# Performance work log

Hardware: AMD Instinct MI355X
Metric: run time of the kernel (lower is better)

Reference implementation:

```python
import jax, jax.numpy as jnp
import numpy as np

B, N, H = 32, 2048, 256          # batch, num_docs, hidden_dim
F_HEADS = 8                      # config.dynamic_fusion_heads
NH = 8                           # num_heads inside each nn.MultiheadAttention
STEPS = 3                        # config.meta_adaptation_steps


def setup_inputs() -> dict:
    key = jax.random.key(0)
    ks = jax.random.split(key, 10)
    s = 0.02
    return {
        "query": jax.random.normal(ks[0], (B, H), jnp.float32),
        "retrieved_docs": jax.random.normal(ks[1], (B, N, H), jnp.float32),
        "causal_weights": jax.random.uniform(ks[2], (B, N, 1), jnp.float32),
        "context_history": jax.random.normal(ks[3], (B, H), jnp.float32),
        # per-fusion-head MultiheadAttention params (torch layout: in_proj [3H,H])
        "in_proj_w": jax.random.normal(ks[4], (F_HEADS, 3 * H, H), jnp.float32) * s,
        "in_proj_b": jnp.zeros((F_HEADS, 3 * H), jnp.float32),
        "out_proj_w": jax.random.normal(ks[5], (F_HEADS, H, H), jnp.float32) * s,
        "out_proj_b": jnp.zeros((F_HEADS, H), jnp.float32),
        "strategy_w": jax.random.normal(ks[6], (F_HEADS, H), jnp.float32) * s,
        "strategy_b": jnp.zeros((F_HEADS,), jnp.float32),
        "meta_params": jax.random.normal(ks[7], (STEPS, H, H), jnp.float32) * 0.02,
    }


def _mha_qlen1(q, kv, Wi, bi, Wo, bo):
    # q: [B,H] (query length 1), kv: [B,N,H]. Torch MHA semantics, batch_first.
    Wq, Wk, Wv = jnp.split(Wi, 3, axis=0)
    bq, bk, bv = jnp.split(bi, 3)
    dh = H // NH
    qh = (q @ Wq.T + bq).reshape(B, NH, dh)
    kh = (kv @ Wk.T + bk).reshape(B, N, NH, dh)
    vh = (kv @ Wv.T + bv).reshape(B, N, NH, dh)
    scores = jnp.einsum('bhd,bnhd->bhn', qh, kh) / jnp.sqrt(jnp.float32(dh))
    attn = jax.nn.softmax(scores, axis=-1)
    ctx = jnp.einsum('bhn,bnhd->bhd', attn, vh).reshape(B, H)
    return ctx @ Wo.T + bo


def reference(query, retrieved_docs, causal_weights, context_history,
              in_proj_w, in_proj_b, out_proj_w, out_proj_b,
              strategy_w, strategy_b, meta_params):
    # causal weighting of retrieved docs (shared across all fusion heads)
    weighted_docs = retrieved_docs * causal_weights  # [B,N,H]

    # batch all 8 fusion heads' cross-attention in one vmapped pass -> [F,B,H]
    heads_out = jax.vmap(
        lambda Wi, bi, Wo, bo: _mha_qlen1(query, weighted_docs, Wi, bi, Wo, bo)
    )(in_proj_w, in_proj_b, out_proj_w, out_proj_b)

    # sequential residual meta-adaptation steps (same matrices for every head)
    for i in range(STEPS):
        heads_out = heads_out + heads_out @ meta_params[i]

    # strategy-weighted combine of fusion heads
    strategy = jax.nn.softmax(query @ strategy_w.T + strategy_b, axis=-1)  # [B,F]
    return jnp.einsum('fbh,bf->bh', heads_out, strategy)  # [B,H]
```

## Files before the change

### kernel.cpp

```cpp
#include <hip/hip_runtime.h>
#include <hip/hip_bf16.h>


#define B_ 32
#define N_ 2048
#define H_ 256
#define F_ 8
#define FH_ 64
#define NCH_ 16
#define NCHK_ 2

typedef unsigned short u16;
typedef __attribute__((ext_vector_type(8))) short bf16x8;
typedef __attribute__((ext_vector_type(4))) float f32x4;
#define MFMA(a, b, c) __builtin_amdgcn_mfma_f32_16x16x32_bf16((a), (b), (c), 0, 0, 0)

__device__ __forceinline__ u16 f2b(float x) {
  unsigned u = __builtin_bit_cast(unsigned, x);
  return (u16)((u + 0x7fffu + ((u >> 16) & 1u)) >> 16);
}
__device__ __forceinline__ float b2f(u16 h) {
  unsigned u = ((unsigned)h) << 16;
  return __builtin_bit_cast(float, u);
}
__device__ __forceinline__ bf16x8 ld8b(const float* p) {
  float4 v0 = *(const float4*)p, v1 = *(const float4*)(p + 4);
  bf16x8 a;
  a[0] = f2b(v0.x); a[1] = f2b(v0.y); a[2] = f2b(v0.z); a[3] = f2b(v0.w);
  a[4] = f2b(v1.x); a[5] = f2b(v1.y); a[6] = f2b(v1.z); a[7] = f2b(v1.w);
  return a;
}

static constexpr size_t UB_U     = 0;
static constexpr size_t UB_W     = 1048576;
static constexpr size_t UB_L     = 3145728;
static constexpr size_t UB_STRAT = 3153920;
static constexpr size_t UB_MT    = 3154944;

#define SMEM_BYTES 52224

__device__ __forceinline__ void dev_k1(char* smem, int f, int hf, int bh,
    const float* __restrict__ query, const float* __restrict__ ipw,
    const float* __restrict__ ipb, const float* __restrict__ stw,
    const float* __restrict__ stb, u16* __restrict__ u, float* __restrict__ strat)
{
  const int tid = threadIdx.x, L = tid & 63, w = tid >> 6;
  const int khi = L >> 4, col = L & 15;
  u16* sW2 = (u16*)smem;
  u16* qhh = (u16*)(smem + 36864);
  u16* qhl = (u16*)(smem + 41216);
  float* slog = (float*)(smem + 45568);

  const int bg = bh * 16 + col;

  bf16x8 qf[8];
  #pragma unroll
  for (int ks = 0; ks < 8; ++ks)
    qf[ks] = ld8b(&query[(size_t)bg * H_ + ks * 32 + khi * 8]);

  if (f == 0 && hf == 0 && w == 0) {
    f32x4 sacc = (f32x4){0.f, 0.f, 0.f, 0.f};
    #pragma unroll
    for (int ks = 0; ks < 8; ++ks) {
      bf16x8 a = (bf16x8){0,0,0,0,0,0,0,0};
      if (col < 8) a = ld8b(&stw[(size_t)col * H_ + ks * 32 + khi * 8]);
      sacc = MFMA(a, qf[ks], sacc);
    }
    if (khi < 2) {
      #pragma unroll
      for (int r = 0; r < 4; ++r) {
        int i = khi * 4 + r;
        slog[col * 8 + i] = sacc[r] + stb[i];
      }
    }
  }

  bf16x8 aq[8];
  #pragma unroll
  for (int ks = 0; ks < 8; ++ks)
    aq[ks] = ld8b(&ipw[((size_t)(f * 768) + hf * 128 + w * 16 + col) * H_ + ks * 32 + khi * 8]);
  f32x4 qacc = (f32x4){0.f, 0.f, 0.f, 0.f};
  #pragma unroll
  for (int ks = 0; ks < 8; ++ks)
    qacc = MFMA(aq[ks], qf[ks], qacc);
  {
    int r0 = w * 16 + khi * 4;
    float4 bq = *(const float4*)&ipb[f * 768 + hf * 128 + r0];
    float v0 = qacc[0] + bq.x, v1 = qacc[1] + bq.y;
    float v2 = qacc[2] + bq.z, v3 = qacc[3] + bq.w;
    ushort4 hs = make_ushort4(f2b(v0), f2b(v1), f2b(v2), f2b(v3));
    ushort4 ls = make_ushort4(f2b(v0 - b2f(hs.x)), f2b(v1 - b2f(hs.y)),
                              f2b(v2 - b2f(hs.z)), f2b(v3 - b2f(hs.w)));
    *(ushort4*)&qhh[col * 136 + r0] = hs;
    *(ushort4*)&qhl[col * 136 + r0] = ls;
  }
  __syncthreads();

  if (f == 0 && hf == 0 && tid < 16) {
    float mx = slog[tid * 8];
    #pragma unroll
    for (int i = 1; i < F_; ++i) mx = fmaxf(mx, slog[tid * 8 + i]);
    float s = 0.f, e[F_];
    #pragma unroll
    for (int i = 0; i < F_; ++i) { e[i] = __expf(slog[tid * 8 + i] - mx); s += e[i]; }
    #pragma unroll
    for (int i = 0; i < F_; ++i) strat[(bh * 16 + tid) * F_ + i] = e[i] / s;
  }

  const float scale = 0.17677669529663687f;
  #pragma unroll
  for (int hp = 0; hp < 2; ++hp) {
    #pragma unroll
    for (int p = 0; p < 8; ++p) {
      int gid = tid + 512 * p;
      int dr = gid >> 6, jq = (gid & 63) * 4;
      float4 v = *(const float4*)&ipw[((size_t)(f * 768 + 256) + hf * 128 + hp * 64 + dr) * H_ + jq];
      float vv[4] = {v.x, v.y, v.z, v.w};
      #pragma unroll
      for (int e2 = 0; e2 < 4; ++e2) {
        int j = jq + e2;
        int m = ((((j >> 4) & 3) ^ ((j >> 2) & 3)) << 3);
        sW2[j * 72 + (dr ^ m)] = f2b(vv[e2]);
      }
    }
    __syncthreads();
    #pragma unroll
    for (int e = 0; e < 2; ++e) {
      #pragma unroll
      for (int q = 0; q < 2; ++q) {
        int jt = w * 2 + q;
        bf16x8 a = *(const bf16x8*)&sW2[(jt * 16 + col) * 72 + e * 32
                                        + ((khi ^ (jt & 3) ^ (col >> 2)) << 3)];
        int rl = (hp * 2 + e) * 32 + khi * 8;
        bf16x8 bhf = *(const bf16x8*)&qhh[col * 136 + rl];
        bf16x8 blf = *(const bf16x8*)&qhl[col * 136 + rl];
        f32x4 acc = (f32x4){0.f, 0.f, 0.f, 0.f};
        acc = MFMA(a, bhf, acc);
        acc = MFMA(a, blf, acc);
        int j0 = jt * 16 + khi * 4;
        ushort4 us = make_ushort4(f2b(acc[0] * scale), f2b(acc[1] * scale),
                                  f2b(acc[2] * scale), f2b(acc[3] * scale));
        *(ushort4*)&u[((size_t)(bg * 64) + f * 8 + hf * 4 + hp * 2 + e) * H_ + j0] = us;
      }
    }
    __syncthreads();
  }
}

__device__ __forceinline__ void dev_meta(char* smem, int bid2,
    const float* __restrict__ meta, u16* __restrict__ metaT)
{
  const int tid = threadIdx.x;
  const int s = bid2 >> 3, x0 = (bid2 & 7) * 32;
  u16* sT = (u16*)smem;
  #pragma unroll
  for (int p = 0; p < 4; ++p) {
    int idx = tid + 512 * p;
    int r = idx >> 3, xq = (idx & 7) * 4;
    float4 v = *(const float4*)&meta[((size_t)(s * 256) + r) * 256 + x0 + xq];
    sT[(xq + 0) * 264 + r] = f2b(v.x);
    sT[(xq + 1) * 264 + r] = f2b(v.y);
    sT[(xq + 2) * 264 + r] = f2b(v.z);
    sT[(xq + 3) * 264 + r] = f2b(v.w);
  }
  __syncthreads();
  #pragma unroll
  for (int p = 0; p < 2; ++p) {
    int idx = tid + 512 * p;
    int x = idx >> 5, rq = (idx & 31) * 8;
    bf16x8 v = *(bf16x8*)&sT[x * 264 + rq];
    *(bf16x8*)&metaT[((size_t)(s * 256) + x0 + x) * 256 + rq] = v;
  }
}

__device__ __forceinline__ void dev_k4(char* smem, int ns, int b,
    const float* __restrict__ docs, const float* __restrict__ cw,
    const u16* __restrict__ u, float* __restrict__ wbuf, float* __restrict__ lbuf)
{
  const int n0 = ns * 128;
  const int tid = threadIdx.x, L = tid & 63, w = tid >> 6;
  const int khi = L >> 4, col = L & 15;
  const int ft = w & 3, nt0 = (w >> 2) * 2;

  u16* sdu  = (u16*)smem;
  u16* phu  = (u16*)(smem + 33792);
  u16* plou = (u16*)(smem + 43008);

  bf16x8 uf[8];
  #pragma unroll
  for (int ks = 0; ks < 8; ++ks)
    uf[ks] = *(const bf16x8*)&u[((size_t)(b * 64) + ft * 16 + col) * H_ + ks * 32 + khi * 8];

  float4 dv[8];
  #pragma unroll
  for (int p = 0; p < 8; ++p) {
    int idx = tid + 512 * p;
    int n = idx >> 6, jq = (idx & 63) * 4;
    dv[p] = *(const float4*)&docs[((size_t)(b * N_) + n0 + n) * H_ + jq];
  }
  #pragma unroll
  for (int p = 0; p < 8; ++p) {
    int idx = tid + 512 * p;
    int n = idx >> 6, jq = (idx & 63) * 4;
    *(ushort4*)&sdu[n * 264 + (jq ^ (((n >> 3) & 3) << 4))] =
        make_ushort4(f2b(dv[p].x), f2b(dv[p].y), f2b(dv[p].z), f2b(dv[p].w));
  }
  __syncthreads();

  f32x4 acc2[4][2];
  #pragma unroll
  for (int mt = 0; mt < 4; ++mt)
    #pragma unroll
    for (int jt = 0; jt < 2; ++jt) acc2[mt][jt] = (f32x4){0.f, 0.f, 0.f, 0.f};
  float eacc[4] = {0.f, 0.f, 0.f, 0.f};

  for (int nc = 0; nc < NCHK_; ++nc) {
    if (nc < NCHK_ - 1) {
      #pragma unroll
      for (int p = 0; p < 8; ++p) {
        int idx = tid + 512 * p;
        int n = idx >> 6, jq = (idx & 63) * 4;
        dv[p] = *(const float4*)&docs[((size_t)(b * N_) + n0 + (nc + 1) * 64 + n) * H_ + jq];
      }
    }
    f32x4 sc0 = (f32x4){0.f, 0.f, 0.f, 0.f}, sc1 = sc0;
    const int nr0 = nt0 * 16 + col, nr1 = (nt0 + 1) * 16 + col;
    const int sw0 = ((nr0 >> 3) & 3) << 4, sw1 = ((nr1 >> 3) & 3) << 4;
    #pragma unroll
    for (int ks = 0; ks < 8; ++ks) {
      bf16x8 b0 = *(const bf16x8*)&sdu[nr0 * 264 + ((ks * 32 + khi * 8) ^ sw0)];
      bf16x8 b1 = *(const bf16x8*)&sdu[nr1 * 264 + ((ks * 32 + khi * 8) ^ sw1)];
      sc0 = MFMA(uf[ks], b0, sc0);
      sc1 = MFMA(uf[ks], b1, sc1);
    }
    {
      int ng = n0 + nc * 64 + nt0 * 16 + col;
      float cv0 = cw[(size_t)b * N_ + ng];
      float cv1 = cw[(size_t)b * N_ + ng + 16];
      #pragma unroll
      for (int r = 0; r < 4; ++r) {
        int fh = ft * 16 + khi * 4 + r;
        float ex0 = __expf(sc0[r] * cv0);
        float ex1 = __expf(sc1[r] * cv1);
        eacc[r] += ex0 + ex1;
        float p0 = ex0 * cv0, p1 = ex1 * cv1;
        u16 h0 = f2b(p0), h1 = f2b(p1);
        phu [fh * 72 + nt0 * 16 + col]       = h0;
        plou[fh * 72 + nt0 * 16 + col]       = f2b(p0 - b2f(h0));
        phu [fh * 72 + (nt0 + 1) * 16 + col] = h1;
        plou[fh * 72 + (nt0 + 1) * 16 + col] = f2b(p1 - b2f(h1));
      }
    }
    __syncthreads();

    #pragma unroll
    for (int kk = 0; kk < 2; ++kk) {
      #pragma unroll
      for (int jt = 0; jt < 2; ++jt) {
        int j = w * 32 + jt * 16 + col;
        bf16x8 bb;
        #pragma unroll
        for (int jj = 0; jj < 8; ++jj)
          bb[jj] = (short)sdu[(kk * 32 + khi * 8 + jj) * 264 + (j ^ (khi << 4))];
        #pragma unroll
        for (int mt = 0; mt < 4; ++mt) {
          bf16x8 ah = *(const bf16x8*)&phu [(mt * 16 + col) * 72 + kk * 32 + khi * 8];
          bf16x8 al = *(const bf16x8*)&plou[(mt * 16 + col) * 72 + kk * 32 + khi * 8];
          acc2[mt][jt] = MFMA(ah, bb, acc2[mt][jt]);
          acc2[mt][jt] = MFMA(al, bb, acc2[mt][jt]);
        }
      }
    }
    __syncthreads();

    if (nc < NCHK_ - 1) {
      #pragma unroll
      for (int p = 0; p < 8; ++p) {
        int idx = tid + 512 * p;
        int n = idx >> 6, jq = (idx & 63) * 4;
        *(ushort4*)&sdu[n * 264 + (jq ^ (((n >> 3) & 3) << 4))] =
            make_ushort4(f2b(dv[p].x), f2b(dv[p].y), f2b(dv[p].z), f2b(dv[p].w));
      }
      __syncthreads();
    }
  }
  #pragma unroll
  for (int mt = 0; mt < 4; ++mt)
    #pragma unroll
    for (int jt = 0; jt < 2; ++jt)
      #pragma unroll
      for (int r = 0; r < 4; ++r) {
        int fh = mt * 16 + khi * 4 + r;
        int j = w * 32 + jt * 16 + col;
        atomicAdd(&wbuf[((size_t)(b * 64) + fh) * H_ + j], acc2[mt][jt][r]);
      }
  #pragma unroll
  for (int r = 0; r < 4; ++r) {
    float e = eacc[r];
    e += __shfl_xor(e, 1, 64);
    e += __shfl_xor(e, 2, 64);
    e += __shfl_xor(e, 4, 64);
    e += __shfl_xor(e, 8, 64);
    if (col == 0)
      atomicAdd(&lbuf[(size_t)(b * 64) + ft * 16 + khi * 4 + r], e);
  }
}

__device__ __forceinline__ void dev_k5(char* smem, int f, int b0,
    const float* __restrict__ ipw, const float* __restrict__ ipb,
    const float* __restrict__ opw, const float* __restrict__ opb,
    const u16* __restrict__ metaT, const float* __restrict__ wbuf,
    const float* __restrict__ lbuf, const float* __restrict__ strat,
    float* __restrict__ out)
{
  const int tid = threadIdx.x, L = tid & 63, w = tid >> 6;
  const int khi = L >> 4, col = L & 15;

  u16* XAh = (u16*)smem;
  u16* XAl = (u16*)(smem + 8448);
  u16* XBh = (u16*)(smem + 16896);
  u16* XBl = (u16*)(smem + 25344);

  bf16x8 av[2][8];
  #pragma unroll
  for (int mt = 0; mt < 2; ++mt)
    #pragma unroll
    for (int ks = 0; ks < 8; ++ks)
      av[mt][ks] = ld8b(&ipw[((size_t)(f * 768 + 512) + w * 32 + mt * 16 + col) * H_
                             + ks * 32 + khi * 8]);
  const size_t wrow = ((size_t)((b0 + col) * 64) + f * 8 + w) * H_;
  const float li = 1.f / lbuf[(size_t)((b0 + col) * 64) + f * 8 + w];
  f32x4 cacc0 = (f32x4){0.f, 0.f, 0.f, 0.f};
  f32x4 cacc1 = (f32x4){0.f, 0.f, 0.f, 0.f};
  #pragma unroll
  for (int ks = 0; ks < 8; ++ks) {
    const float* p = &wbuf[wrow + ks * 32 + khi * 8];
    float4 v0 = *(const float4*)p, v1 = *(const float4*)(p + 4);
    float vv[8] = {v0.x, v0.y, v0.z, v0.w, v1.x, v1.y, v1.z, v1.w};
    bf16x8 bh, bl;
    #pragma unroll
    for (int e = 0; e < 8; ++e) {
      float x = vv[e] * li;
      u16 h = f2b(x);
      bh[e] = (short)h;
      bl[e] = (short)f2b(x - b2f(h));
    }
    cacc0 = MFMA(av[0][ks], bh, cacc0); cacc0 = MFMA(av[0][ks], bl, cacc0);
    cacc1 = MFMA(av[1][ks], bh, cacc1); cacc1 = MFMA(av[1][ks], bl, cacc1);
  }
  #pragma unroll
  for (int mt = 0; mt < 2; ++mt) {
    f32x4 cv = mt ? cacc1 : cacc0;
    #pragma unroll
    for (int r = 0; r < 4; ++r) {
      int d = mt * 16 + khi * 4 + r;
      float vv = cv[r] + ipb[f * 768 + 512 + w * 32 + d];
      u16 hi = f2b(vv);
      XAh[col * 264 + w * 32 + d] = hi;
      XAl[col * 264 + w * 32 + d] = f2b(vv - b2f(hi));
    }
  }

  bf16x8 bw[2][8];
  #pragma unroll
  for (int q = 0; q < 2; ++q)
    #pragma unroll
    for (int ks = 0; ks < 8; ++ks)
      bw[q][ks] = ld8b(&opw[((size_t)(f * 256) + (w * 2 + q) * 16 + col) * H_
                            + ks * 32 + khi * 8]);
  __syncthreads();

  f32x4 hr0, hr1;
  {
    float bo0 = opb[f * 256 + (w * 2 + 0) * 16 + col];
    float bo1 = opb[f * 256 + (w * 2 + 1) * 16 + col];
    hr0 = (f32x4){bo0, bo0, bo0, bo0};
    hr1 = (f32x4){bo1, bo1, bo1, bo1};
  }
  #pragma unroll
  for (int ks = 0; ks < 8; ++ks) {
    bf16x8 ah = *(const bf16x8*)&XAh[col * 264 + ks * 32 + khi * 8];
    bf16x8 al = *(const bf16x8*)&XAl[col * 264 + ks * 32 + khi * 8];
    hr0 = MFMA(ah, bw[0][ks], hr0); hr0 = MFMA(al, bw[0][ks], hr0);
    hr1 = MFMA(ah, bw[1][ks], hr1); hr1 = MFMA(al, bw[1][ks], hr1);
  }

  auto spill = [&](u16* Oh, u16* Ol) {
    #pragma unroll
    for (int q = 0; q < 2; ++q) {
      f32x4 hv = q ? hr1 : hr0;
      int x = (w * 2 + q) * 16 + col;
      #pragma unroll
      for (int r = 0; r < 4; ++r) {
        u16 hi = f2b(hv[r]);
        Oh[(khi * 4 + r) * 264 + x] = hi;
        Ol[(khi * 4 + r) * 264 + x] = f2b(hv[r] - b2f(hi));
      }
    }
  };
  auto meta_mm = [&](const u16* Ah_, const u16* Al_, int s) {
    f32x4 n0 = hr0, n1 = hr1;
    #pragma unroll
    for (int ks = 0; ks < 8; ++ks) {
      bf16x8 ah = *(const bf16x8*)&Ah_[col * 264 + ks * 32 + khi * 8];
      bf16x8 al = *(const bf16x8*)&Al_[col * 264 + ks * 32 + khi * 8];
      const u16* mrow = &metaT[((size_t)(s * 256) + (w * 2) * 16 + col) * 256 + ks * 32 + khi * 8];
      bf16x8 m0 = *(const bf16x8*)mrow;
      bf16x8 m1 = *(const bf16x8*)(mrow + 16 * 256);
      n0 = MFMA(ah, m0, n0); n0 = MFMA(al, m0, n0);
      n1 = MFMA(ah, m1, n1); n1 = MFMA(al, m1, n1);
    }
    hr0 = n0; hr1 = n1;
  };

  spill(XBh, XBl);
  __syncthreads();
  meta_mm(XBh, XBl, 0);
  spill(XAh, XAl);
  __syncthreads();
  meta_mm(XAh, XAl, 1);
  spill(XBh, XBl);
  __syncthreads();
  meta_mm(XBh, XBl, 2);

  #pragma unroll
  for (int q = 0; q < 2; ++q) {
    f32x4 hv = q ? hr1 : hr0;
    int x = (w * 2 + q) * 16 + col;
    #pragma unroll
    for (int r = 0; r < 4; ++r) {
      int b = khi * 4 + r;
      float sv = strat[(b0 + b) * F_ + f];
      atomicAdd(&out[(size_t)(b0 + b) * H_ + x], sv * hv[r]);
    }
  }
}

__global__ __launch_bounds__(512) void k1_all(
    const float* __restrict__ query, const float* __restrict__ ipw,
    const float* __restrict__ ipb, const float* __restrict__ stw,
    const float* __restrict__ stb, const float* __restrict__ meta,
    u16* __restrict__ u, u16* __restrict__ metaT, float* __restrict__ strat,
    float* __restrict__ wbuf, float* __restrict__ out)
{
  __shared__ __align__(16) char smem[SMEM_BYTES];
  const int bid = blockIdx.x, tid = threadIdx.x;
  if (bid < 32) {
    dev_k1(smem, bid >> 2, (bid >> 1) & 1, bid & 1, query, ipw, ipb, stw, stb, u, strat);
  } else if (bid < 56) {
    dev_meta(smem, bid - 32, meta, metaT);
  } else {
    int zb = bid - 56;
    float4 z4 = make_float4(0.f, 0.f, 0.f, 0.f);
    float4* z = (float4*)wbuf;
    for (int i = zb * 512 + tid; i < 131584; i += 16 * 512) z[i] = z4;
    if (zb < 4) ((float4*)out)[zb * 512 + tid] = z4;
  }
}

__global__ __launch_bounds__(512) void k4_sep(
    const float* __restrict__ docs, const float* __restrict__ cw,
    const u16* __restrict__ u, float* __restrict__ wbuf, float* __restrict__ lbuf)
{
  __shared__ __align__(16) char smem[SMEM_BYTES];
  dev_k4(smem, blockIdx.x, blockIdx.y, docs, cw, u, wbuf, lbuf);
}

__global__ __launch_bounds__(512) void k5_sep(
    const float* __restrict__ ipw, const float* __restrict__ ipb,
    const float* __restrict__ opw, const float* __restrict__ opb,
    const u16* __restrict__ metaT, const float* __restrict__ wbuf,
    const float* __restrict__ lbuf, const float* __restrict__ strat,
    float* __restrict__ out)
{
  __shared__ __align__(16) char smem[SMEM_BYTES];
  dev_k5(smem, blockIdx.x & 7, (blockIdx.x >> 3) * 16,
         ipw, ipb, opw, opb, metaT, wbuf, lbuf, strat, out);
}

extern "C" void kernel_launch(void* const* d_in, const int* in_sizes, int n_in,
                              void* d_out, int out_size, void* d_ws, size_t ws_size,
                              hipStream_t stream) {
  const float* query = (const float*)d_in[0];
  const float* docs  = (const float*)d_in[1];
  const float* cw    = (const float*)d_in[2];
  const float* ipw   = (const float*)d_in[4];
  const float* ipb   = (const float*)d_in[5];
  const float* opw   = (const float*)d_in[6];
  const float* opb   = (const float*)d_in[7];
  const float* stw   = (const float*)d_in[8];
  const float* stb   = (const float*)d_in[9];
  const float* meta  = (const float*)d_in[10];
  float* out = (float*)d_out;

  char* base = (char*)d_ws;
  u16*   u     = (u16*)(base + UB_U);
  float* wbuf  = (float*)(base + UB_W);
  float* lbuf  = (float*)(base + UB_L);
  float* strat = (float*)(base + UB_STRAT);
  u16*   metaT = (u16*)(base + UB_MT);

  k1_all<<<dim3(72), 512, 0, stream>>>(query, ipw, ipb, stw, stb, meta,
                                       u, metaT, strat, wbuf, out);
  k4_sep<<<dim3(NCH_, B_), 512, 0, stream>>>(docs, cw, u, wbuf, lbuf);
  k5_sep<<<dim3(16), 512, 0, stream>>>(ipw, ipb, opw, opb, metaT, wbuf, lbuf, strat, out);
}
```

Before: 195.7 us.

## Fuse doc-attention and output kernels via last-block ticket, halve chunk count

Merges the separate doc-attention and output-projection kernels into one launch. Each batch group of 16 takes a global atomic ticket after its blocks finish, and the last eight arrivals run the output-projection stage. It also doubles the per-block doc chunk (8 chunks of 256 instead of 16 of 128), which halves the grid to 256 blocks. The aim is to remove one launch and the tail gap between kernels, at the cost of fewer blocks in flight and serialized tail work on the final blocks.

```diff
diff --git a/kernel.cpp b/kernel.cpp
--- a/kernel.cpp
+++ b/kernel.cpp
@@ -7,8 +7,8 @@
 #define H_ 256
 #define F_ 8
 #define FH_ 64
-#define NCH_ 16
-#define NCHK_ 2
+#define NCH_ 8
+#define NCHK_ 4
 
 typedef unsigned short u16;
 typedef __attribute__((ext_vector_type(8))) short bf16x8;
@@ -36,6 +36,7 @@
 static constexpr size_t UB_L     = 3145728;
 static constexpr size_t UB_STRAT = 3153920;
 static constexpr size_t UB_MT    = 3154944;
+static constexpr size_t UB_TK    = 3548160;
 
 #define SMEM_BYTES 52224
 
@@ -177,7 +178,7 @@
     const float* __restrict__ docs, const float* __restrict__ cw,
     const u16* __restrict__ u, float* __restrict__ wbuf, float* __restrict__ lbuf)
 {
-  const int n0 = ns * 128;
+  const int n0 = ns * 256;
   const int tid = threadIdx.x, L = tid & 63, w = tid >> 6;
   const int khi = L >> 4, col = L & 15;
   const int ft = w & 3, nt0 = (w >> 2) * 2;
@@ -441,7 +442,7 @@
     const float* __restrict__ ipb, const float* __restrict__ stw,
     const float* __restrict__ stb, const float* __restrict__ meta,
     u16* __restrict__ u, u16* __restrict__ metaT, float* __restrict__ strat,
-    float* __restrict__ wbuf, float* __restrict__ out)
+    float* __restrict__ wbuf, float* __restrict__ out, unsigned* __restrict__ tk)
 {
   __shared__ __align__(16) char smem[SMEM_BYTES];
   const int bid = blockIdx.x, tid = threadIdx.x;
@@ -455,27 +456,36 @@
     float4* z = (float4*)wbuf;
     for (int i = zb * 512 + tid; i < 131584; i += 16 * 512) z[i] = z4;
     if (zb < 4) ((float4*)out)[zb * 512 + tid] = z4;
-  }
-}
-
-__global__ __launch_bounds__(512) void k4_sep(
+    if (zb == 0 && tid < 2) tk[tid] = 0u;
+  }
+}
+
+__global__ __launch_bounds__(512) void k4k5_fused(
     const float* __restrict__ docs, const float* __restrict__ cw,
-    const u16* __restrict__ u, float* __restrict__ wbuf, float* __restrict__ lbuf)
+    const u16* __restrict__ u, float* __restrict__ wbuf, float* __restrict__ lbuf,
+    const float* __restrict__ ipw, const float* __restrict__ ipb,
+    const float* __restrict__ opw, const float* __restrict__ opb,
+    const u16* __restrict__ metaT, const float* __restrict__ strat,
+    float* __restrict__ out, unsigned* __restrict__ tk)
 {
   __shared__ __align__(16) char smem[SMEM_BYTES];
-  dev_k4(smem, blockIdx.x, blockIdx.y, docs, cw, u, wbuf, lbuf);
-}
-
-__global__ __launch_bounds__(512) void k5_sep(
-    const float* __restrict__ ipw, const float* __restrict__ ipb,
-    const float* __restrict__ opw, const float* __restrict__ opb,
-    const u16* __restrict__ metaT, const float* __restrict__ wbuf,
-    const float* __restrict__ lbuf, const float* __restrict__ strat,
-    float* __restrict__ out)
-{
-  __shared__ __align__(16) char smem[SMEM_BYTES];
-  dev_k5(smem, blockIdx.x & 7, (blockIdx.x >> 3) * 16,
-         ipw, ipb, opw, opb, metaT, wbuf, lbuf, strat, out);
+  __shared__ unsigned tkt;
+  const int ns = blockIdx.x, b = blockIdx.y;
+
+  dev_k4(smem, ns, b, docs, cw, u, wbuf, lbuf);
+
+  __threadfence();
+  __syncthreads();
+  if (threadIdx.x == 0)
+    tkt = __hip_atomic_fetch_add(&tk[b >> 4], 1u, __ATOMIC_ACQ_REL,
+                                 __HIP_MEMORY_SCOPE_AGENT);
+  __syncthreads();
+  unsigned t = tkt;
+  if (t >= 120u) {
+    __threadfence();
+    dev_k5(smem, (int)(t - 120u), (b >> 4) * 16,
+           ipw, ipb, opw, opb, metaT, wbuf, lbuf, strat, out);
+  }
 }
 
 extern "C" void kernel_launch(void* const* d_in, const int* in_sizes, int n_in,
@@ -494,14 +504,16 @@
   float* out = (float*)d_out;
 
   char* base = (char*)d_ws;
-  u16*   u     = (u16*)(base + UB_U);
-  float* wbuf  = (float*)(base + UB_W);
-  float* lbuf  = (float*)(base + UB_L);
-  float* strat = (float*)(base + UB_STRAT);
-  u16*   metaT = (u16*)(base + UB_MT);
+  u16*      u     = (u16*)(base + UB_U);
+  float*    wbuf  = (float*)(base + UB_W);
+  float*    lbuf  = (float*)(base + UB_L);
+  float*    strat = (float*)(base + UB_STRAT);
+  u16*      metaT = (u16*)(base + UB_MT);
+  unsigned* tk    = (unsigned*)(base + UB_TK);
 
   k1_all<<<dim3(72), 512, 0, stream>>>(query, ipw, ipb, stw, stb, meta,
-                                       u, metaT, strat, wbuf, out);
-  k4_sep<<<dim3(NCH_, B_), 512, 0, stream>>>(docs, cw, u, wbuf, lbuf);
-  k5_sep<<<dim3(16), 512, 0, stream>>>(ipw, ipb, opw, opb, metaT, wbuf, lbuf, strat, out);
-}
+                                       u, metaT, strat, wbuf, out, tk);
+  k4k5_fused<<<dim3(NCH_, B_), 512, 0, stream>>>(docs, cw, u, wbuf, lbuf,
+                                                 ipw, ipb, opw, opb, metaT,
+                                                 strat, out, tk);
+}
```

After: 225.0 us. +15.0%, slower.
